# Performance work log

Measured on AMD Instinct MI355X. Metric: run time of the kernel, lower is better.

Reference implementation:

```python
import jax, jax.numpy as jnp
import numpy as np

EPS = 1e-12

def setup_inputs() -> dict:
    key = jax.random.key(0)
    kp, kq = jax.random.split(key)
    B, N, M = 64, 512, 512
    p = jax.random.normal(kp, (2, B, N, 4), dtype=jnp.float32)  # generated jets (complex)
    q = jax.random.normal(kq, (2, B, M, 4), dtype=jnp.float32)  # target jets (complex)
    return {"p": p, "q": q}

def _normsq_cplx(d):
    # d: (2, B, N, M, 4) complex 4-vector differences; Minkowski metric (+,-,-,-)
    re_sq = d[0] * d[0]
    m_real = 2.0 * re_sq[..., 0] - re_sq.sum(axis=-1)          # (B,N,M)
    pq = d[0] * d[1]
    m_im = 2.0 * (2.0 * pq[..., 0] - pq.sum(axis=-1))          # (B,N,M)
    return jnp.sqrt(m_real * m_real + m_im * m_im + EPS)

def reference(p, q):
    # pairwise difference tensor: (2, B, N, M, 4)
    d = p[:, :, :, None, :] - q[:, :, None, :, :]
    dist = _normsq_cplx(d)                                     # (B, N, M)
    min_pq = dist.min(axis=-1)                                 # (B, N)
    min_qp = dist.min(axis=-2)                                 # (B, M)
    return jnp.sum(min_pq) + jnp.sum(min_qp)
```

## Files before the change

kernel.cpp:

```cpp
#include <hip/hip_runtime.h>
#include <math.h>

#define EPS 1e-12f

constexpr int Bn = 64;
constexpr int Np = 512;
constexpr int OSPLIT = 4;
constexpr int OWN = Np / OSPLIT;
constexpr int TPB = 256;
constexpr int KSPLIT = 4;
constexpr int KCH = Np / KSPLIT;

__global__ __launch_bounds__(TPB) void chamfer_min_kernel(
        const float* __restrict__ p, const float* __restrict__ q,
        float* __restrict__ partial) {
    const int b    = blockIdx.x;
    const int pass = blockIdx.y;
    const int oc   = blockIdx.z;
    const float* A = (pass == 0) ? p : q;
    const float* L = (pass == 0) ? q : p;

    const int t  = threadIdx.x;
    const int ot = t & 63;
    const int kh = __builtin_amdgcn_readfirstlane(t >> 6);

    const float4* are = (const float4*)(A + (size_t)b * Np * 4);
    const float4* aim = (const float4*)(A + (size_t)(Bn + b) * Np * 4);
    const int o = oc * OWN + ot * 2;
    const float4 pr0 = are[o], pr1 = are[o + 1];
    const float4 pi0 = aim[o], pi1 = aim[o + 1];

    const float4* lre = (const float4*)(L + (size_t)b * Np * 4);
    const float4* lim = (const float4*)(L + (size_t)(Bn + b) * Np * 4);

    float s0 = 3.4e38f, s1 = 3.4e38f;
    const int k0 = kh * KCH;
    #pragma unroll 8
    for (int k = k0; k < k0 + KCH; ++k) {
        const float4 qr = lre[k];
        const float4 qi = lim[k];
        {
            float drx = pr0.x - qr.x, dry = pr0.y - qr.y;
            float drz = pr0.z - qr.z, drw = pr0.w - qr.w;
            float dix = pi0.x - qi.x, diy = pi0.y - qi.y;
            float diz = pi0.z - qi.z, diw = pi0.w - qi.w;
            float mr  = drx*drx - dry*dry - drz*drz - drw*drw;
            float mi  = drx*dix - dry*diy - drz*diz - drw*diw;
            float mi2 = mi + mi;
            float s   = mr*mr + mi2*mi2;
            s0 = fminf(s0, s);
        }
        {
            float drx = pr1.x - qr.x, dry = pr1.y - qr.y;
            float drz = pr1.z - qr.z, drw = pr1.w - qr.w;
            float dix = pi1.x - qi.x, diy = pi1.y - qi.y;
            float diz = pi1.z - qi.z, diw = pi1.w - qi.w;
            float mr  = drx*drx - dry*dry - drz*drz - drw*drw;
            float mi  = drx*dix - dry*diy - drz*diz - drw*diw;
            float mi2 = mi + mi;
            float s   = mr*mr + mi2*mi2;
            s1 = fminf(s1, s);
        }
    }

    __shared__ float2 sred[TPB];
    sred[t] = make_float2(s0, s1);
    __syncthreads();
    if (t < 64) {
        float2 a  = sred[t];
        float2 b2 = sred[t + 64];
        float2 c  = sred[t + 128];
        float2 d  = sred[t + 192];
        float m0 = fminf(fminf(a.x, b2.x), fminf(c.x, d.x));
        float m1 = fminf(fminf(a.y, b2.y), fminf(c.y, d.y));
        float v = sqrtf(m0 + EPS) + sqrtf(m1 + EPS);
        #pragma unroll
        for (int off = 32; off > 0; off >>= 1)
            v += __shfl_down(v, off, 64);
        if (t == 0)
            partial[(((size_t)pass * Bn + b) * OSPLIT) + oc] = v;
    }
}

__global__ __launch_bounds__(256) void final_sum_kernel(
        const float* __restrict__ partial, float* __restrict__ outp) {
    __shared__ float red[256];
    const int t = threadIdx.x;
    red[t] = partial[t] + partial[t + 256];
    __syncthreads();
    for (int s = 128; s > 0; s >>= 1) {
        if (t < s) red[t] += red[t + s];
        __syncthreads();
    }
    if (t == 0) outp[0] = red[0];
}

extern "C" void kernel_launch(void* const* d_in, const int* in_sizes, int n_in,
                              void* d_out, int out_size, void* d_ws, size_t ws_size,
                              hipStream_t stream) {
    const float* p = (const float*)d_in[0];
    const float* q = (const float*)d_in[1];
    float* out     = (float*)d_out;
    float* partial = (float*)d_ws;

    dim3 grid(Bn, 2, OSPLIT);
    chamfer_min_kernel<<<grid, TPB, 0, stream>>>(p, q, partial);
    final_sum_kernel<<<1, 256, 0, stream>>>(partial, out);
}
```

Before: 22.17 us.

## Fuse final reduction via last-block atomic counter and double K-split threads

Removes the separate final-sum kernel launch: each block writes its partial sum, bumps a global atomic counter, and the last block to arrive reduces all 512 partials. It also doubles threads per block to 512 with an 8-way split of the inner loop, giving more waves per block and shorter per-thread loops. A memset of the counter is added before the launch, and the work per thread drops while the shared-memory reduction grows.

```diff
diff --git a/kernel.cpp b/kernel.cpp
--- a/kernel.cpp
+++ b/kernel.cpp
@@ -7,13 +7,15 @@
 constexpr int Np = 512;
 constexpr int OSPLIT = 4;
 constexpr int OWN = Np / OSPLIT;
-constexpr int TPB = 256;
-constexpr int KSPLIT = 4;
+constexpr int TPB = 512;
+constexpr int KSPLIT = 8;
 constexpr int KCH = Np / KSPLIT;
+constexpr int NBLK = Bn * 2 * OSPLIT;
 
 __global__ __launch_bounds__(TPB) void chamfer_min_kernel(
         const float* __restrict__ p, const float* __restrict__ q,
-        float* __restrict__ partial) {
+        float* __restrict__ partial, unsigned* __restrict__ counter,
+        float* __restrict__ outp) {
     const int b    = blockIdx.x;
     const int pass = blockIdx.y;
     const int oc   = blockIdx.z;
@@ -47,8 +49,7 @@
             float mr  = drx*drx - dry*dry - drz*drz - drw*drw;
             float mi  = drx*dix - dry*diy - drz*diz - drw*diw;
             float mi2 = mi + mi;
-            float s   = mr*mr + mi2*mi2;
-            s0 = fminf(s0, s);
+            s0 = fminf(s0, mr*mr + mi2*mi2);
         }
         {
             float drx = pr1.x - qr.x, dry = pr1.y - qr.y;
@@ -58,41 +59,49 @@
             float mr  = drx*drx - dry*dry - drz*drz - drw*drw;
             float mi  = drx*dix - dry*diy - drz*diz - drw*diw;
             float mi2 = mi + mi;
-            float s   = mr*mr + mi2*mi2;
-            s1 = fminf(s1, s);
+            s1 = fminf(s1, mr*mr + mi2*mi2);
         }
     }
 
     __shared__ float2 sred[TPB];
+    __shared__ float  red[TPB];
+    __shared__ int    sflag;
     sred[t] = make_float2(s0, s1);
     __syncthreads();
+
     if (t < 64) {
-        float2 a  = sred[t];
-        float2 b2 = sred[t + 64];
-        float2 c  = sred[t + 128];
-        float2 d  = sred[t + 192];
-        float m0 = fminf(fminf(a.x, b2.x), fminf(c.x, d.x));
-        float m1 = fminf(fminf(a.y, b2.y), fminf(c.y, d.y));
+        float m0 = s0, m1 = s1;
+        #pragma unroll
+        for (int w = 1; w < KSPLIT; ++w) {
+            float2 v = sred[t + w * 64];
+            m0 = fminf(m0, v.x);
+            m1 = fminf(m1, v.y);
+        }
         float v = sqrtf(m0 + EPS) + sqrtf(m1 + EPS);
         #pragma unroll
         for (int off = 32; off > 0; off >>= 1)
             v += __shfl_down(v, off, 64);
-        if (t == 0)
-            partial[(((size_t)pass * Bn + b) * OSPLIT) + oc] = v;
+        if (t == 0) {
+            const int bid = (oc * 2 + pass) * Bn + b;
+            partial[bid] = v;
+            __threadfence();
+            unsigned old = __hip_atomic_fetch_add(counter, 1u,
+                              __ATOMIC_ACQ_REL, __HIP_MEMORY_SCOPE_AGENT);
+            sflag = (old == NBLK - 1) ? 1 : 0;
+        }
     }
-}
+    __syncthreads();
 
-__global__ __launch_bounds__(256) void final_sum_kernel(
-        const float* __restrict__ partial, float* __restrict__ outp) {
-    __shared__ float red[256];
-    const int t = threadIdx.x;
-    red[t] = partial[t] + partial[t + 256];
-    __syncthreads();
-    for (int s = 128; s > 0; s >>= 1) {
-        if (t < s) red[t] += red[t + s];
+    if (sflag) {
+        __threadfence();
+        red[t] = partial[t];
         __syncthreads();
+        for (int s = TPB / 2; s > 0; s >>= 1) {
+            if (t < s) red[t] += red[t + s];
+            __syncthreads();
+        }
+        if (t == 0) outp[0] = red[0];
     }
-    if (t == 0) outp[0] = red[0];
 }
 
 extern "C" void kernel_launch(void* const* d_in, const int* in_sizes, int n_in,
@@ -100,10 +109,11 @@
                               hipStream_t stream) {
     const float* p = (const float*)d_in[0];
     const float* q = (const float*)d_in[1];
-    float* out     = (float*)d_out;
-    float* partial = (float*)d_ws;
+    float* out       = (float*)d_out;
+    float* partial   = (float*)d_ws;
+    unsigned* counter = (unsigned*)((char*)d_ws + NBLK * sizeof(float));
 
+    hipMemsetAsync(counter, 0, sizeof(unsigned), stream);
     dim3 grid(Bn, 2, OSPLIT);
-    chamfer_min_kernel<<<grid, TPB, 0, stream>>>(p, q, partial);
-    final_sum_kernel<<<1, 256, 0, stream>>>(partial, out);
+    chamfer_min_kernel<<<grid, TPB, 0, stream>>>(p, q, partial, counter, out);
 }
```

Result: slower. 42.95 us (+93.7%).

## Pack pairwise distance math into float2 vectors and double k-split waves

Applied to the files above, without the earlier changes.

Rewrites the per-pair distance computation with two-wide float vectors so the compiler can emit packed FP32 instructions (v_pk_fma/v_pk_mul), roughly halving ALU instruction count for the two owned points. It also doubles the block to 512 threads with an 8-way split over the inner loop dimension, giving more waves per block to hide load latency and shortening each wave's loop. The reduction now folds eight partial minima per lane instead of four, at the cost of more shared memory and fewer blocks resident per CU.

```diff
diff --git a/kernel.cpp b/kernel.cpp
--- a/kernel.cpp
+++ b/kernel.cpp
@@ -3,12 +3,14 @@
 
 #define EPS 1e-12f
 
+typedef float v2f __attribute__((ext_vector_type(2)));
+
 constexpr int Bn = 64;
 constexpr int Np = 512;
 constexpr int OSPLIT = 4;
 constexpr int OWN = Np / OSPLIT;
-constexpr int TPB = 256;
-constexpr int KSPLIT = 4;
+constexpr int TPB = 512;
+constexpr int KSPLIT = 8;
 constexpr int KCH = Np / KSPLIT;
 
 __global__ __launch_bounds__(TPB) void chamfer_min_kernel(
@@ -27,53 +29,43 @@
     const float4* are = (const float4*)(A + (size_t)b * Np * 4);
     const float4* aim = (const float4*)(A + (size_t)(Bn + b) * Np * 4);
     const int o = oc * OWN + ot * 2;
-    const float4 pr0 = are[o], pr1 = are[o + 1];
-    const float4 pi0 = aim[o], pi1 = aim[o + 1];
+    const float4 a0 = are[o], a1 = are[o + 1];
+    const float4 b0 = aim[o], b1 = aim[o + 1];
+    const v2f prx = {a0.x, a1.x}, pry = {a0.y, a1.y};
+    const v2f prz = {a0.z, a1.z}, prw = {a0.w, a1.w};
+    const v2f pix = {b0.x, b1.x}, piy = {b0.y, b1.y};
+    const v2f piz = {b0.z, b1.z}, piw = {b0.w, b1.w};
 
     const float4* lre = (const float4*)(L + (size_t)b * Np * 4);
     const float4* lim = (const float4*)(L + (size_t)(Bn + b) * Np * 4);
 
-    float s0 = 3.4e38f, s1 = 3.4e38f;
+    v2f smin = {3.4e38f, 3.4e38f};
     const int k0 = kh * KCH;
     #pragma unroll 8
     for (int k = k0; k < k0 + KCH; ++k) {
         const float4 qr = lre[k];
         const float4 qi = lim[k];
-        {
-            float drx = pr0.x - qr.x, dry = pr0.y - qr.y;
-            float drz = pr0.z - qr.z, drw = pr0.w - qr.w;
-            float dix = pi0.x - qi.x, diy = pi0.y - qi.y;
-            float diz = pi0.z - qi.z, diw = pi0.w - qi.w;
-            float mr  = drx*drx - dry*dry - drz*drz - drw*drw;
-            float mi  = drx*dix - dry*diy - drz*diz - drw*diw;
-            float mi2 = mi + mi;
-            float s   = mr*mr + mi2*mi2;
-            s0 = fminf(s0, s);
-        }
-        {
-            float drx = pr1.x - qr.x, dry = pr1.y - qr.y;
-            float drz = pr1.z - qr.z, drw = pr1.w - qr.w;
-            float dix = pi1.x - qi.x, diy = pi1.y - qi.y;
-            float diz = pi1.z - qi.z, diw = pi1.w - qi.w;
-            float mr  = drx*drx - dry*dry - drz*drz - drw*drw;
-            float mi  = drx*dix - dry*diy - drz*diz - drw*diw;
-            float mi2 = mi + mi;
-            float s   = mr*mr + mi2*mi2;
-            s1 = fminf(s1, s);
-        }
+        v2f drx = prx - qr.x, dry = pry - qr.y;
+        v2f drz = prz - qr.z, drw = prw - qr.w;
+        v2f dix = pix - qi.x, diy = piy - qi.y;
+        v2f diz = piz - qi.z, diw = piw - qi.w;
+        v2f mr  = drx*drx - dry*dry - drz*drz - drw*drw;
+        v2f mi  = drx*dix - dry*diy - drz*diz - drw*diw;
+        v2f mi2 = mi + mi;
+        v2f s   = mr*mr + mi2*mi2;
+        smin = __builtin_elementwise_min(smin, s);
     }
 
-    __shared__ float2 sred[TPB];
-    sred[t] = make_float2(s0, s1);
+    __shared__ v2f sred[TPB];
+    sred[t] = smin;
     __syncthreads();
+
     if (t < 64) {
-        float2 a  = sred[t];
-        float2 b2 = sred[t + 64];
-        float2 c  = sred[t + 128];
-        float2 d  = sred[t + 192];
-        float m0 = fminf(fminf(a.x, b2.x), fminf(c.x, d.x));
-        float m1 = fminf(fminf(a.y, b2.y), fminf(c.y, d.y));
-        float v = sqrtf(m0 + EPS) + sqrtf(m1 + EPS);
+        v2f m = smin;
+        #pragma unroll
+        for (int w = 1; w < KSPLIT; ++w)
+            m = __builtin_elementwise_min(m, sred[t + w * 64]);
+        float v = sqrtf(m.x + EPS) + sqrtf(m.y + EPS);
         #pragma unroll
         for (int off = 32; off > 0; off >>= 1)
             v += __shfl_down(v, off, 64);
```

After: 21.37 us. 3.6% less time.
